# Optimization experiments

Hardware: AMD Instinct MI355X
Metric: run time of the kernel (lower is better)

Reference implementation:

```python
import jax, jax.numpy as jnp
import numpy as np

EMBED_DIM = 768
D_K = 64
B, S = 4, 4096


def setup_inputs() -> dict:
    key = jax.random.key(0)
    ks = jax.random.split(key, 7)
    scale = 1.0 / np.sqrt(EMBED_DIM)
    return {
        "x": jax.random.normal(ks[0], (B, S, EMBED_DIM), dtype=jnp.float32),
        "Wq": jax.random.normal(ks[1], (EMBED_DIM, D_K), dtype=jnp.float32) * scale,
        "bq": jax.random.normal(ks[2], (D_K,), dtype=jnp.float32) * 0.01,
        "Wk": jax.random.normal(ks[3], (EMBED_DIM, D_K), dtype=jnp.float32) * scale,
        "bk": jax.random.normal(ks[4], (D_K,), dtype=jnp.float32) * 0.01,
        "Wv": jax.random.normal(ks[5], (EMBED_DIM, D_K), dtype=jnp.float32) * scale,
        "bv": jax.random.normal(ks[6], (D_K,), dtype=jnp.float32) * 0.01,
    }


def reference(x, Wq, bq, Wk, bk, Wv, bv):
    # Linear projections: [B, S, E] @ [E, d_k] + bias -> [B, S, d_k]
    q = jnp.einsum("bse,ed->bsd", x, Wq) + bq
    k = jnp.einsum("bse,ed->bsd", x, Wk) + bk
    v = jnp.einsum("bse,ed->bsd", x, Wv) + bv
    # Scaled dot-product attention; scores: [B, S, S]
    scores = jnp.einsum("bqd,bkd->bqk", q, k) / jnp.sqrt(jnp.asarray(D_K, x.dtype))
    attn = jax.nn.softmax(scores, axis=-1)
    return jnp.einsum("bqk,bkd->bqd", attn, v)
```

## Files before the change

kernel.cpp:

```cpp
#include <hip/hip_runtime.h>

typedef _Float16 f16;
typedef f16 f16x2 __attribute__((ext_vector_type(2)));
typedef f16 f16x4 __attribute__((ext_vector_type(4)));
typedef f16 f16x8 __attribute__((ext_vector_type(8)));
typedef float f32x4 __attribute__((ext_vector_type(4)));

#define MFMA32(A, B, C) __builtin_amdgcn_mfma_f32_16x16x32_f16(A, B, C, 0, 0, 0)
#define MFMA16(A, B, C) __builtin_amdgcn_mfma_f32_16x16x16f16(A, B, C, 0, 0, 0)

#define QSCALE (0.125f * 1.44269504088896340736f)
#define MSHIFT 10.0f

__device__ __forceinline__ f16x2 pkrtz(float a, float b) {
  return __builtin_bit_cast(f16x2, __builtin_amdgcn_cvt_pkrtz(a, b));
}
__device__ __forceinline__ void nts(f16* p, f16x8 v) {
  __builtin_nontemporal_store(v, (f16x8*)p);
}
__device__ __forceinline__ f16x8 ntl(const f16* p) {
  return __builtin_nontemporal_load((const f16x8*)p);
}

__global__ __launch_bounds__(256) void wtrans_kernel(
    const float* __restrict__ Wq, const float* __restrict__ Wk,
    const float* __restrict__ Wv, f16* __restrict__ Wt) {
  __shared__ float T[64][65];
  const int t = threadIdx.x;
  const int kt = blockIdx.x;
  const int z = blockIdx.y;
  const float* W = (z == 0) ? Wq : ((z == 1) ? Wk : Wv);

  {
    const int kl = t >> 2, c0 = (t & 3) * 16;
    const float* wp = W + (kt * 64 + kl) * 64 + c0;
    float4 v0 = *(const float4*)wp;
    float4 v1 = *(const float4*)(wp + 4);
    float4 v2 = *(const float4*)(wp + 8);
    float4 v3 = *(const float4*)(wp + 12);
    float* Tr = &T[kl][c0];
    Tr[0] = v0.x; Tr[1] = v0.y; Tr[2] = v0.z; Tr[3] = v0.w;
    Tr[4] = v1.x; Tr[5] = v1.y; Tr[6] = v1.z; Tr[7] = v1.w;
    Tr[8] = v2.x; Tr[9] = v2.y; Tr[10] = v2.z; Tr[11] = v2.w;
    Tr[12] = v3.x; Tr[13] = v3.y; Tr[14] = v3.z; Tr[15] = v3.w;
  }
  __syncthreads();
  {
    const int n = t >> 2, k0 = (t & 3) * 16;
    union { f16x2 h2[8]; f16x8 h8[2]; } u;
#pragma unroll
    for (int i = 0; i < 8; i++)
      u.h2[i] = pkrtz(T[k0 + 2 * i][n], T[k0 + 2 * i + 1][n]);
    f16* dst = Wt + (z * 64 + n) * 768 + kt * 64 + k0;
    *(f16x8*)dst = u.h8[0];
    *(f16x8*)(dst + 8) = u.h8[1];
  }
}

__global__ __launch_bounds__(256, 4) void proj_kernel(
    const float* __restrict__ x, const f16* __restrict__ Wt,
    const float* __restrict__ bq, const float* __restrict__ bk,
    const float* __restrict__ bv, f16* __restrict__ qo, f16* __restrict__ ko,
    f16* __restrict__ vt) {
  __shared__ f16 Xs[32][72];
  __shared__ f16 Ws[192][72];

  const int t = threadIdx.x;
  const int w = t >> 6;
  const int lane = t & 63;
  const int ln = lane & 15;
  const int quad = lane >> 4;
  const int mh = w & 1;
  const int nh = w >> 1;
  const int r0 = blockIdx.x * 32;

  f32x4 acc[6];
#pragma unroll
  for (int i = 0; i < 6; i++) acc[i] = (f32x4){0.f, 0.f, 0.f, 0.f};

  const int xsr = t >> 3, xsc = (t & 7) * 8;
  const int wsr = t >> 2, wsc = (t & 3) * 16;
  const float* xr = x + (r0 + xsr) * 768 + xsc;
  const f16* wr = Wt + wsr * 768 + wsc;

  float4 xa0, xa1;
  f16x8 wf[3][2];
  xa0 = *(const float4*)xr;
  xa1 = *(const float4*)(xr + 4);
#pragma unroll
  for (int p = 0; p < 3; p++) {
    wf[p][0] = *(const f16x8*)(wr + p * 64 * 768);
    wf[p][1] = *(const f16x8*)(wr + p * 64 * 768 + 8);
  }

  for (int kc = 0; kc < 12; kc++) {
    __syncthreads();
    {
      union { f16x2 h2[4]; f16x8 h8; } u;
      u.h2[0] = pkrtz(xa0.x, xa0.y); u.h2[1] = pkrtz(xa0.z, xa0.w);
      u.h2[2] = pkrtz(xa1.x, xa1.y); u.h2[3] = pkrtz(xa1.z, xa1.w);
      *(f16x8*)&Xs[xsr][xsc] = u.h8;
#pragma unroll
      for (int p = 0; p < 3; p++) {
        *(f16x8*)&Ws[p * 64 + wsr][wsc] = wf[p][0];
        *(f16x8*)&Ws[p * 64 + wsr][wsc + 8] = wf[p][1];
      }
    }
    if (kc + 1 < 12) {
      const float* xp = xr + (kc + 1) * 64;
      xa0 = *(const float4*)xp;
      xa1 = *(const float4*)(xp + 4);
      const f16* wp = wr + (kc + 1) * 64;
#pragma unroll
      for (int p = 0; p < 3; p++) {
        wf[p][0] = *(const f16x8*)(wp + p * 64 * 768);
        wf[p][1] = *(const f16x8*)(wp + p * 64 * 768 + 8);
      }
    }
    __syncthreads();

    f16x8 a0 = *(const f16x8*)&Xs[mh * 16 + ln][quad * 8];
    f16x8 a1 = *(const f16x8*)&Xs[mh * 16 + ln][32 + quad * 8];
#pragma unroll
    for (int nt = 0; nt < 6; nt++) {
      f16x8 b0 = *(const f16x8*)&Ws[nh * 96 + nt * 16 + ln][quad * 8];
      f16x8 b1 = *(const f16x8*)&Ws[nh * 96 + nt * 16 + ln][32 + quad * 8];
      acc[nt] = MFMA32(a0, b0, acc[nt]);
      acc[nt] = MFMA32(a1, b1, acc[nt]);
    }
  }

  const int rowg = r0 + mh * 16 + quad * 4;
  if (nh == 0) {
#pragma unroll
    for (int nt = 0; nt < 4; nt++) {
      int d = nt * 16 + ln;
      float bb = bq[d];
#pragma unroll
      for (int r = 0; r < 4; r++)
        qo[(rowg + r) * 64 + d] = (f16)((acc[nt][r] + bb) * QSCALE);
    }
#pragma unroll
    for (int nt = 4; nt < 6; nt++) {
      int d = nt * 16 + ln - 64;
      float bb = bk[d];
#pragma unroll
      for (int r = 0; r < 4; r++)
        ko[(rowg + r) * 64 + d] = (f16)(acc[nt][r] + bb);
    }
  } else {
#pragma unroll
    for (int nt = 0; nt < 2; nt++) {
      int d = 32 + nt * 16 + ln;
      float bb = bk[d];
#pragma unroll
      for (int r = 0; r < 4; r++)
        ko[(rowg + r) * 64 + d] = (f16)(acc[nt][r] + bb);
    }
    const int bidx = rowg >> 12;
    const int sb = rowg & 4095;
#pragma unroll
    for (int nt = 2; nt < 6; nt++) {
      int dv = nt * 16 + ln - 32;
      float bb = bv[dv];
      f16x4 hv;
#pragma unroll
      for (int r = 0; r < 4; r++) hv[r] = (f16)(acc[nt][r] + bb);
      *(f16x4*)&vt[((bidx * 64 + dv) << 12) + sb] = hv;
    }
  }
}

__global__ __launch_bounds__(512, 4) void attn_kernel(
    const f16* __restrict__ qo, const f16* __restrict__ ko,
    const f16* __restrict__ vt, f16* __restrict__ po, float* __restrict__ pl) {
  constexpr int CS = 8, NK = 4096 / CS;
  __shared__ f16 Ksh[64][76];
  __shared__ f16 Vsh[64][76];

  const int t = threadIdx.x;
  const int w = t >> 6;
  const int lane = t & 63;
  const int ln = lane & 15;
  const int quad = lane >> 4;
  const int bid = blockIdx.x;
  const int c = bid & 7;
  const int qb = bid >> 3;
  const int b = qb >> 4;

  f16x8 bq0[2], bq1[2];
#pragma unroll
  for (int h = 0; h < 2; h++) {
    const int qoff = (qb * 256 + w * 32 + h * 16 + ln) * 64 + quad * 8;
    bq0[h] = *(const f16x8*)(qo + qoff);
    bq1[h] = *(const f16x8*)(qo + qoff + 32);
  }

  f32x4 o[2][4];
#pragma unroll
  for (int h = 0; h < 2; h++)
#pragma unroll
    for (int i = 0; i < 4; i++) o[h][i] = (f32x4){0.f, 0.f, 0.f, 0.f};
  float l_s[2] = {0.f, 0.f};

  const int rr = t >> 3;
  const int cc = (t & 7) * 8;
  const f16* kbase = ko + (b * 4096 + c * NK) * 64;
  const f16* vbase = vt + b * 64 * 4096 + c * NK;

  f16x8 kreg = *(const f16x8*)(kbase + rr * 64 + cc);
  f16x8 vreg = *(const f16x8*)(vbase + rr * 4096 + cc);

  for (int kt = 0; kt < NK / 64; kt++) {
    __syncthreads();
    *(f16x8*)&Ksh[rr][cc] = kreg;
    *(f16x8*)&Vsh[rr][cc] = vreg;
    __syncthreads();

    if (kt + 1 < NK / 64) {
      const int ks1 = (kt + 1) * 64;
      kreg = *(const f16x8*)(kbase + (ks1 + rr) * 64 + cc);
      vreg = *(const f16x8*)(vbase + rr * 4096 + ks1 + cc);
    }

    f16x8 ka[4], kb[4];
#pragma unroll
    for (int nt = 0; nt < 4; nt++) {
      ka[nt] = *(const f16x8*)&Ksh[nt * 16 + ln][quad * 8];
      kb[nt] = *(const f16x8*)&Ksh[nt * 16 + ln][32 + quad * 8];
    }

#pragma unroll
    for (int h = 0; h < 2; h++) {
      f32x4 st[4];
#pragma unroll
      for (int i = 0; i < 4; i++) st[i] = (f32x4){0.f, 0.f, 0.f, 0.f};
#pragma unroll
      for (int nt = 0; nt < 4; nt++) {
        st[nt] = MFMA32(ka[nt], bq0[h], st[nt]);
        st[nt] = MFMA32(kb[nt], bq1[h], st[nt]);
      }

      f16x4 pa[4];
#pragma unroll
      for (int nt = 0; nt < 4; nt++) {
        float p0 = exp2f(st[nt][0] - MSHIFT);
        float p1 = exp2f(st[nt][1] - MSHIFT);
        float p2 = exp2f(st[nt][2] - MSHIFT);
        float p3 = exp2f(st[nt][3] - MSHIFT);
        l_s[h] += (p0 + p1) + (p2 + p3);
        union { f16x2 h2[2]; f16x4 h4; } u;
        u.h2[0] = pkrtz(p0, p1);
        u.h2[1] = pkrtz(p2, p3);
        pa[nt] = u.h4;
      }

#pragma unroll
      for (int nt = 0; nt < 4; nt++)
#pragma unroll
        for (int dt = 0; dt < 4; dt++) {
          f16x4 bv = *(const f16x4*)&Vsh[dt * 16 + ln][nt * 16 + quad * 4];
          o[h][dt] = MFMA16(pa[nt], bv, o[h][dt]);
        }
    }
  }

#pragma unroll
  for (int h = 0; h < 2; h++) {
    const int g = qb * 16 + w * 2 + h;
    union { f16x2 h2[8]; f16x8 h8[2]; } u;
#pragma unroll
    for (int dt = 0; dt < 4; dt++) {
      u.h2[dt * 2] = pkrtz(o[h][dt][0], o[h][dt][1]);
      u.h2[dt * 2 + 1] = pkrtz(o[h][dt][2], o[h][dt][3]);
    }
    f16* p = po + (((size_t)c * 1024 + g) * 64 + lane) * 16;
    nts(p, u.h8[0]);
    nts(p + 8, u.h8[1]);
    float rs = l_s[h];
    rs += __shfl_xor(rs, 16);
    rs += __shfl_xor(rs, 32);
    if (quad == 0) pl[c * 16384 + g * 16 + ln] = rs;
  }
}

__global__ __launch_bounds__(256) void merge_kernel(
    const f16* __restrict__ po, const float* __restrict__ pl,
    float* __restrict__ out) {
  const int t = threadIdx.x;
  const int w = t >> 6;
  const int lane = t & 63;
  const int ln = lane & 15;
  const int quad = lane >> 4;
  const int g = blockIdx.x * 4 + w;

  f32x4 o2[4];
#pragma unroll
  for (int i = 0; i < 4; i++) o2[i] = (f32x4){0.f, 0.f, 0.f, 0.f};
  float den[4] = {0.f, 0.f, 0.f, 0.f};

#pragma unroll
  for (int c = 0; c < 8; c++) {
#pragma unroll
    for (int r = 0; r < 4; r++)
      den[r] += pl[c * 16384 + g * 16 + quad * 4 + r];
    const f16* p = po + (((size_t)c * 1024 + g) * 64 + lane) * 16;
    f16x8 l0 = ntl(p);
    f16x8 l1 = ntl(p + 8);
#pragma unroll
    for (int dt = 0; dt < 2; dt++)
#pragma unroll
      for (int r = 0; r < 4; r++) {
        o2[dt][r] += (float)l0[dt * 4 + r];
        o2[dt + 2][r] += (float)l1[dt * 4 + r];
      }
  }

  const int orow = g * 16 + quad * 4;
#pragma unroll
  for (int r = 0; r < 4; r++) {
    float inv = 1.0f / den[r];
#pragma unroll
    for (int dt = 0; dt < 4; dt++)
      out[(orow + r) * 64 + dt * 16 + ln] = o2[dt][r] * inv;
  }
}

extern "C" void kernel_launch(void* const* d_in, const int* in_sizes, int n_in,
                              void* d_out, int out_size, void* d_ws,
                              size_t ws_size, hipStream_t stream) {
  const float* x = (const float*)d_in[0];
  const float* Wq = (const float*)d_in[1];
  const float* bq = (const float*)d_in[2];
  const float* Wk = (const float*)d_in[3];
  const float* bk = (const float*)d_in[4];
  const float* Wv = (const float*)d_in[5];
  const float* bv = (const float*)d_in[6];
  float* out = (float*)d_out;

  char* ws = (char*)d_ws;
  f16* Wt = (f16*)ws;
  f16* qo = (f16*)(ws + 294912);
  f16* ko = (f16*)(ws + 294912 + 2097152);
  f16* vt = (f16*)(ws + 294912 + 2 * 2097152);
  const size_t base = 6586368;

  f16* po = (f16*)(ws + base);
  float* pl = (float*)(ws + base + (size_t)8 * 16384 * 64 * 2);

  wtrans_kernel<<<dim3(12, 3), dim3(256), 0, stream>>>(Wq, Wk, Wv, Wt);
  proj_kernel<<<dim3(512), dim3(256), 0, stream>>>(x, Wt, bq, bk, bv, qo, ko, vt);
  attn_kernel<<<dim3(512), dim3(512), 0, stream>>>(qo, ko, vt, po, pl);
  merge_kernel<<<dim3(256), dim3(256), 0, stream>>>(po, pl, out);
}
```

Baseline: 144.9 us.

## Halve projection k-chunk for occupancy and load K fragments directly from global

```diff
diff --git a/kernel.cpp b/kernel.cpp
--- a/kernel.cpp
+++ b/kernel.cpp
@@ -57,13 +57,13 @@
   }
 }
 
-__global__ __launch_bounds__(256, 4) void proj_kernel(
+__global__ __launch_bounds__(256, 6) void proj_kernel(
     const float* __restrict__ x, const f16* __restrict__ Wt,
     const float* __restrict__ bq, const float* __restrict__ bk,
     const float* __restrict__ bv, f16* __restrict__ qo, f16* __restrict__ ko,
     f16* __restrict__ vt) {
-  __shared__ f16 Xs[32][72];
-  __shared__ f16 Ws[192][72];
+  __shared__ f16 Xs[32][40];
+  __shared__ f16 Ws[192][40];
 
   const int t = threadIdx.x;
   const int w = t >> 6;
@@ -78,55 +78,40 @@
 #pragma unroll
   for (int i = 0; i < 6; i++) acc[i] = (f32x4){0.f, 0.f, 0.f, 0.f};
 
-  const int xsr = t >> 3, xsc = (t & 7) * 8;
-  const int wsr = t >> 2, wsc = (t & 3) * 16;
+  const int xsr = t >> 3, xsc = (t & 7) * 4;
+  const int wsr = t >> 2, wsc = (t & 3) * 8;
   const float* xr = x + (r0 + xsr) * 768 + xsc;
   const f16* wr = Wt + wsr * 768 + wsc;
 
-  float4 xa0, xa1;
-  f16x8 wf[3][2];
-  xa0 = *(const float4*)xr;
-  xa1 = *(const float4*)(xr + 4);
-#pragma unroll
-  for (int p = 0; p < 3; p++) {
-    wf[p][0] = *(const f16x8*)(wr + p * 64 * 768);
-    wf[p][1] = *(const f16x8*)(wr + p * 64 * 768 + 8);
-  }
-
-  for (int kc = 0; kc < 12; kc++) {
+  float4 xa = *(const float4*)xr;
+  f16x8 wf[3];
+#pragma unroll
+  for (int p = 0; p < 3; p++) wf[p] = *(const f16x8*)(wr + p * 64 * 768);
+
+  for (int kc = 0; kc < 24; kc++) {
     __syncthreads();
     {
-      union { f16x2 h2[4]; f16x8 h8; } u;
-      u.h2[0] = pkrtz(xa0.x, xa0.y); u.h2[1] = pkrtz(xa0.z, xa0.w);
-      u.h2[2] = pkrtz(xa1.x, xa1.y); u.h2[3] = pkrtz(xa1.z, xa1.w);
-      *(f16x8*)&Xs[xsr][xsc] = u.h8;
-#pragma unroll
-      for (int p = 0; p < 3; p++) {
-        *(f16x8*)&Ws[p * 64 + wsr][wsc] = wf[p][0];
-        *(f16x8*)&Ws[p * 64 + wsr][wsc + 8] = wf[p][1];
-      }
-    }
-    if (kc + 1 < 12) {
-      const float* xp = xr + (kc + 1) * 64;
-      xa0 = *(const float4*)xp;
-      xa1 = *(const float4*)(xp + 4);
-      const f16* wp = wr + (kc + 1) * 64;
-#pragma unroll
-      for (int p = 0; p < 3; p++) {
-        wf[p][0] = *(const f16x8*)(wp + p * 64 * 768);
-        wf[p][1] = *(const f16x8*)(wp + p * 64 * 768 + 8);
-      }
+      union { f16x2 h2[2]; f16x4 h4; } u;
+      u.h2[0] = pkrtz(xa.x, xa.y);
+      u.h2[1] = pkrtz(xa.z, xa.w);
+      *(f16x4*)&Xs[xsr][xsc] = u.h4;
+#pragma unroll
+      for (int p = 0; p < 3; p++) *(f16x8*)&Ws[p * 64 + wsr][wsc] = wf[p];
+    }
+    if (kc + 1 < 24) {
+      const float* xp = xr + (kc + 1) * 32;
+      xa = *(const float4*)xp;
+      const f16* wp = wr + (kc + 1) * 32;
+#pragma unroll
+      for (int p = 0; p < 3; p++) wf[p] = *(const f16x8*)(wp + p * 64 * 768);
     }
     __syncthreads();
 
     f16x8 a0 = *(const f16x8*)&Xs[mh * 16 + ln][quad * 8];
-    f16x8 a1 = *(const f16x8*)&Xs[mh * 16 + ln][32 + quad * 8];
 #pragma unroll
     for (int nt = 0; nt < 6; nt++) {
       f16x8 b0 = *(const f16x8*)&Ws[nh * 96 + nt * 16 + ln][quad * 8];
-      f16x8 b1 = *(const f16x8*)&Ws[nh * 96 + nt * 16 + ln][32 + quad * 8];
       acc[nt] = MFMA32(a0, b0, acc[nt]);
-      acc[nt] = MFMA32(a1, b1, acc[nt]);
     }
   }
 
@@ -175,7 +160,6 @@
     const f16* __restrict__ qo, const f16* __restrict__ ko,
     const f16* __restrict__ vt, f16* __restrict__ po, float* __restrict__ pl) {
   constexpr int CS = 8, NK = 4096 / CS;
-  __shared__ f16 Ksh[64][76];
   __shared__ f16 Vsh[64][76];
 
   const int t = threadIdx.x;
@@ -207,27 +191,25 @@
   const int cc = (t & 7) * 8;
   const f16* kbase = ko + (b * 4096 + c * NK) * 64;
   const f16* vbase = vt + b * 64 * 4096 + c * NK;
-
-  f16x8 kreg = *(const f16x8*)(kbase + rr * 64 + cc);
+  const f16* krow = kbase + ln * 64 + quad * 8;
+
   f16x8 vreg = *(const f16x8*)(vbase + rr * 4096 + cc);
 
   for (int kt = 0; kt < NK / 64; kt++) {
     __syncthreads();
-    *(f16x8*)&Ksh[rr][cc] = kreg;
     *(f16x8*)&Vsh[rr][cc] = vreg;
     __syncthreads();
 
     if (kt + 1 < NK / 64) {
-      const int ks1 = (kt + 1) * 64;
-      kreg = *(const f16x8*)(kbase + (ks1 + rr) * 64 + cc);
-      vreg = *(const f16x8*)(vbase + rr * 4096 + ks1 + cc);
-    }
-
+      vreg = *(const f16x8*)(vbase + rr * 4096 + (kt + 1) * 64 + cc);
+    }
+
+    const f16* kp = krow + kt * 64 * 64;
     f16x8 ka[4], kb[4];
 #pragma unroll
     for (int nt = 0; nt < 4; nt++) {
-      ka[nt] = *(const f16x8*)&Ksh[nt * 16 + ln][quad * 8];
-      kb[nt] = *(const f16x8*)&Ksh[nt * 16 + ln][32 + quad * 8];
+      ka[nt] = *(const f16x8*)(kp + nt * 16 * 64);
+      kb[nt] = *(const f16x8*)(kp + nt * 16 * 64 + 32);
     }
 
 #pragma unroll
```

New measurement: 156.5 us. +8.0%, slower.
